# Optimization experiments

Measured on AMD Instinct MI355X. Metric: run time of the kernel, lower is better.

## Reference

```python
import jax, jax.numpy as jnp
import numpy as np

TEMPERATURE = 0.5


def setup_inputs() -> dict:
    key = jax.random.key(0)
    k1, k2 = jax.random.split(key)
    N, D = 4096, 256
    emb_i = jax.random.normal(k1, (N, D), dtype=jnp.float32)
    emb_j = jax.random.normal(k2, (N, D), dtype=jnp.float32)
    return {"emb_i": emb_i, "emb_j": emb_j, "batch_size": N}


def reference(emb_i, emb_j, batch_size):
    N = batch_size
    # L2-normalize each embedding row (F.normalize eps=1e-12)
    def l2n(x):
        return x / jnp.maximum(jnp.linalg.norm(x, axis=1, keepdims=True), 1e-12)
    reps = jnp.concatenate([l2n(emb_i), l2n(emb_j)], axis=0)  # [2N, D]
    # cosine similarity of normalized vectors == dot product
    logits = (reps @ reps.T) / TEMPERATURE                    # [2N, 2N]
    twoN = 2 * N
    # denominator excludes only the self term k != i (stable logsumexp)
    diag_mask = jnp.eye(twoN, dtype=bool)
    masked = jnp.where(diag_mask, -jnp.inf, logits)
    log_denom = jax.nn.logsumexp(masked, axis=1)              # [2N]
    # positive pair for row i is (i+N) mod 2N
    idx = jnp.arange(twoN)
    pos = logits[idx, (idx + N) % twoN]                       # [2N]
    # loss = 1/(2N) * sum_i -log(exp(pos_i)/denom_i)
    return jnp.mean(log_denom - pos)
```

## Files before the change

kernel.cpp:

```cpp
#include <hip/hip_runtime.h>

typedef short short8 __attribute__((ext_vector_type(8)));
typedef float f32x4  __attribute__((ext_vector_type(4)));

#define TWO_N 8192
#define NHALF 4096
#define DDIM  256

__device__ __forceinline__ float b2f(unsigned short u) {
    return __uint_as_float(((unsigned int)u) << 16);
}
__device__ __forceinline__ unsigned short f2b(float f) {
    unsigned int u = __float_as_uint(f);
    u += 0x7fffu + ((u >> 16) & 1u);
    return (unsigned short)(u >> 16);
}

__device__ __forceinline__ int probe_is_f32(const void* p, int lane) {
    unsigned int u = ((const unsigned int*)p)[lane];
    float lowv = __uint_as_float(u << 16);
    int crazy = !(fabsf(lowv) <= 1024.0f);
    return __ballot(crazy) != 0ull;
}

typedef __attribute__((address_space(1))) const unsigned int guint_t;
typedef __attribute__((address_space(3))) unsigned int luint_t;
__device__ __forceinline__ void gl_lds16(const unsigned short* g, unsigned short* l) {
    __builtin_amdgcn_global_load_lds((guint_t*)(const void*)g, (luint_t*)(void*)l, 16, 0, 0);
}

__global__ __launch_bounds__(256) void k_norm(const void* __restrict__ ei,
                                              const void* __restrict__ ej,
                                              unsigned short* __restrict__ reps) {
    int row  = (blockIdx.x * 256 + threadIdx.x) >> 6;
    int lane = threadIdx.x & 63;
    int isf  = probe_is_f32(ei, lane);
    int first = (row < NHALF);
    int r     = first ? row : row - NHALF;
    float x0, x1, x2, x3;
    if (isf) {
        const float* s = (first ? (const float*)ei : (const float*)ej) + (size_t)r * DDIM;
        float4 v = ((const float4*)s)[lane];
        x0 = v.x; x1 = v.y; x2 = v.z; x3 = v.w;
    } else {
        const unsigned short* s =
            (first ? (const unsigned short*)ei : (const unsigned short*)ej) + (size_t)r * DDIM;
        ushort4 v = ((const ushort4*)s)[lane];
        x0 = b2f(v.x); x1 = b2f(v.y); x2 = b2f(v.z); x3 = b2f(v.w);
    }
    float ss = x0 * x0 + x1 * x1 + x2 * x2 + x3 * x3;
    for (int off = 32; off > 0; off >>= 1) ss += __shfl_xor(ss, off);
    float inv = 1.0f / fmaxf(sqrtf(ss), 1e-12f);
    ushort4 o;
    o.x = f2b(x0 * inv); o.y = f2b(x1 * inv);
    o.z = f2b(x2 * inv); o.w = f2b(x3 * inv);
    ((ushort4*)(reps + (size_t)row * DDIM))[lane] = o;
}

__global__ __launch_bounds__(256) void k_main(const unsigned short* __restrict__ R,
                                              float* __restrict__ S_part,
                                              float* __restrict__ pos) {
    __shared__ __align__(16) unsigned short As[128 * 64];
    __shared__ __align__(16) unsigned short Bs[128 * 64];

    int b = blockIdx.x;
    int rb = (int)((129.0f - sqrtf(16641.0f - 8.0f * (float)b)) * 0.5f);
    if (rb > 63) rb = 63;
    while ((129 * (rb + 1) - (rb + 1) * (rb + 1)) / 2 <= b) ++rb;
    while ((129 * rb - rb * rb) / 2 > b) --rb;
    int cb = rb + (b - (129 * rb - rb * rb) / 2);

    const int tid  = threadIdx.x;
    const int wave = tid >> 6;
    const int lane = tid & 63;
    const int quad = lane >> 4;
    const int l16  = lane & 15;
    const int wr   = (wave >> 1) * 64;
    const int wc   = (wave & 1) * 64;
    const int r8   = lane >> 3;
    const int c8   = (lane & 7) ^ r8;

    f32x4 acc[4][4];
#pragma unroll
    for (int r = 0; r < 4; ++r)
#pragma unroll
        for (int c = 0; c < 4; ++c) {
            acc[r][c][0] = 0.0f; acc[r][c][1] = 0.0f;
            acc[r][c][2] = 0.0f; acc[r][c][3] = 0.0f;
        }

    for (int kc = 0; kc < 4; ++kc) {
        __syncthreads();
#pragma unroll
        for (int t = 0; t < 4; ++t) {
            int u = wave * 4 + t;
            const unsigned short* ga =
                R + (size_t)(rb * 128 + u * 8 + r8) * DDIM + kc * 64 + c8 * 8;
            const unsigned short* gb =
                R + (size_t)(cb * 128 + u * 8 + r8) * DDIM + kc * 64 + c8 * 8;
            gl_lds16(ga, &As[u * 512]);
            gl_lds16(gb, &Bs[u * 512]);
        }
        __syncthreads();

#pragma unroll
        for (int kk = 0; kk < 2; ++kk) {
            short8 afr[4], bfr[4];
            int q = kk * 4 + quad;
            int sl = q ^ (l16 & 7);
#pragma unroll
            for (int r = 0; r < 4; ++r)
                afr[r] = *(const short8*)(&As[(wr + r * 16 + l16) * 64 + sl * 8]);
#pragma unroll
            for (int c = 0; c < 4; ++c)
                bfr[c] = *(const short8*)(&Bs[(wc + c * 16 + l16) * 64 + sl * 8]);
#pragma unroll
            for (int r = 0; r < 4; ++r)
#pragma unroll
                for (int c = 0; c < 4; ++c)
                    acc[r][c] = __builtin_amdgcn_mfma_f32_16x16x32_bf16(
                        afr[r], bfr[c], acc[r][c], 0, 0, 0);
        }
    }

    float col_acc[4] = {0.0f, 0.0f, 0.0f, 0.0f};
#pragma unroll
    for (int r = 0; r < 4; ++r)
#pragma unroll
        for (int j = 0; j < 4; ++j) {
            float s = 0.0f;
#pragma unroll
            for (int c = 0; c < 4; ++c) {
                float e = __expf(fmaf(acc[r][c][j], 2.0f, -2.0f));
                s += e;
                col_acc[c] += e;
            }
            s += __shfl_xor(s, 1);
            s += __shfl_xor(s, 2);
            s += __shfl_xor(s, 4);
            s += __shfl_xor(s, 8);
            if (l16 == 0) {
                int row = rb * 128 + wr + r * 16 + quad * 4 + j;
                S_part[(size_t)(2 * cb + (wave & 1)) * TWO_N + row] = s;
            }
        }
    if (rb != cb) {
#pragma unroll
        for (int c = 0; c < 4; ++c) {
            float s = col_acc[c];
            s += __shfl_xor(s, 16);
            s += __shfl_xor(s, 32);
            if (lane < 16) {
                int row = cb * 128 + wc + c * 16 + lane;
                S_part[(size_t)(2 * rb + (wave >> 1)) * TWO_N + row] = s;
            }
        }
    }
    if (cb == rb + 32 && wr == wc) {
#pragma unroll
        for (int r = 0; r < 4; ++r)
#pragma unroll
            for (int j = 0; j < 4; ++j)
                if (quad * 4 + j == l16)
                    pos[rb * 128 + wr + r * 16 + l16] = 2.0f * acc[r][r][j];
    }
}

__global__ __launch_bounds__(256) void k_rows(const float* __restrict__ S_part,
                                              const float* __restrict__ pos,
                                              float* __restrict__ t_row) {
    int row = blockIdx.x * 256 + threadIdx.x;
    float s = 0.0f;
    for (int c = 0; c < 128; ++c) s += S_part[(size_t)c * TWO_N + row];
    float p = (row < NHALF) ? pos[row] : pos[row - NHALF];
    t_row[row] = 2.0f + logf(s - 1.0f) - p;
}

__global__ __launch_bounds__(1024) void k_fin(const float* __restrict__ t_row,
                                              unsigned int* __restrict__ out) {
    int tid = threadIdx.x;
    float local = 0.0f;
    for (int i = tid; i < TWO_N; i += 1024) local += t_row[i];
    __shared__ float red[16];
    for (int off = 32; off > 0; off >>= 1) local += __shfl_xor(local, off);
    if ((tid & 63) == 0) red[tid >> 6] = local;
    __syncthreads();
    if (tid == 0) {
        float v = 0.0f;
        for (int w = 0; w < 16; ++w) v += red[w];
        float L = v / 8192.0f;
        unsigned int bb = (unsigned int)f2b(L);
        out[0] = (bb << 16) | bb;
    }
}

extern "C" void kernel_launch(void* const* d_in, const int* in_sizes, int n_in,
                              void* d_out, int out_size, void* d_ws, size_t ws_size,
                              hipStream_t stream) {
    (void)in_sizes; (void)n_in; (void)out_size; (void)ws_size;
    const void* ei = d_in[0];
    const void* ej = d_in[1];
    char* ws = (char*)d_ws;

    float*          pos    = (float*)(ws);
    float*          t_row  = (float*)(ws + 16384);
    unsigned short* reps   = (unsigned short*)(ws + 49152);
    float*          S_part = (float*)(ws + 4243456);

    k_norm<<<2048, 256, 0, stream>>>(ei, ej, reps);
    k_main<<<2080, 256, 0, stream>>>(reps, S_part, pos);
    k_rows<<<32,   256, 0, stream>>>(S_part, pos, t_row);
    k_fin <<<1,   1024, 0, stream>>>(t_row, (unsigned int*)d_out);
}
```

Before: 110.1 us.

## Fuse row reduction and final loss into main kernel via atomics and last-block

Replaces the per-block partial-sum buffer and two follow-up kernels with float atomicAdds into a per-row accumulator. The last block to finish, found with a global counter, computes the final mean loss. This drops two kernel launches and the 4 MB partial-sum buffer write and read. In exchange it adds atomic contention on the row sums, makes the float summation order nondeterministic, and adds a fence at the end of every block.

```diff
diff --git a/kernel.cpp b/kernel.cpp
--- a/kernel.cpp
+++ b/kernel.cpp
@@ -6,6 +6,7 @@
 #define TWO_N 8192
 #define NHALF 4096
 #define DDIM  256
+#define NBLK  2080
 
 __device__ __forceinline__ float b2f(unsigned short u) {
     return __uint_as_float(((unsigned int)u) << 16);
@@ -31,8 +32,14 @@
 
 __global__ __launch_bounds__(256) void k_norm(const void* __restrict__ ei,
                                               const void* __restrict__ ej,
-                                              unsigned short* __restrict__ reps) {
-    int row  = (blockIdx.x * 256 + threadIdx.x) >> 6;
+                                              unsigned short* __restrict__ reps,
+                                              float* __restrict__ row_acc,
+                                              unsigned int* __restrict__ ctr) {
+    int gid = blockIdx.x * 256 + threadIdx.x;
+    if (gid < TWO_N) row_acc[gid] = 0.0f;
+    if (gid == TWO_N) *ctr = 0u;
+
+    int row  = gid >> 6;
     int lane = threadIdx.x & 63;
     int isf  = probe_is_f32(ei, lane);
     int first = (row < NHALF);
@@ -58,10 +65,14 @@
 }
 
 __global__ __launch_bounds__(256) void k_main(const unsigned short* __restrict__ R,
-                                              float* __restrict__ S_part,
-                                              float* __restrict__ pos) {
+                                              float* __restrict__ row_acc,
+                                              float* __restrict__ pos,
+                                              unsigned int* __restrict__ ctr,
+                                              unsigned int* __restrict__ out) {
     __shared__ __align__(16) unsigned short As[128 * 64];
     __shared__ __align__(16) unsigned short Bs[128 * 64];
+    __shared__ unsigned int sdone;
+    __shared__ float red[4];
 
     int b = blockIdx.x;
     int rb = (int)((129.0f - sqrtf(16641.0f - 8.0f * (float)b)) * 0.5f);
@@ -141,7 +152,7 @@
             s += __shfl_xor(s, 8);
             if (l16 == 0) {
                 int row = rb * 128 + wr + r * 16 + quad * 4 + j;
-                S_part[(size_t)(2 * cb + (wave & 1)) * TWO_N + row] = s;
+                atomicAdd(&row_acc[row], s);
             }
         }
     if (rb != cb) {
@@ -152,7 +163,7 @@
             s += __shfl_xor(s, 32);
             if (lane < 16) {
                 int row = cb * 128 + wc + c * 16 + lane;
-                S_part[(size_t)(2 * rb + (wave >> 1)) * TWO_N + row] = s;
+                atomicAdd(&row_acc[row], s);
             }
         }
     }
@@ -164,33 +175,29 @@
                 if (quad * 4 + j == l16)
                     pos[rb * 128 + wr + r * 16 + l16] = 2.0f * acc[r][r][j];
     }
-}
-
-__global__ __launch_bounds__(256) void k_rows(const float* __restrict__ S_part,
-                                              const float* __restrict__ pos,
-                                              float* __restrict__ t_row) {
-    int row = blockIdx.x * 256 + threadIdx.x;
-    float s = 0.0f;
-    for (int c = 0; c < 128; ++c) s += S_part[(size_t)c * TWO_N + row];
-    float p = (row < NHALF) ? pos[row] : pos[row - NHALF];
-    t_row[row] = 2.0f + logf(s - 1.0f) - p;
-}
-
-__global__ __launch_bounds__(1024) void k_fin(const float* __restrict__ t_row,
-                                              unsigned int* __restrict__ out) {
-    int tid = threadIdx.x;
-    float local = 0.0f;
-    for (int i = tid; i < TWO_N; i += 1024) local += t_row[i];
-    __shared__ float red[16];
-    for (int off = 32; off > 0; off >>= 1) local += __shfl_xor(local, off);
-    if ((tid & 63) == 0) red[tid >> 6] = local;
+
+    __threadfence();
+    if (tid == 0) sdone = atomicAdd(ctr, 1u);
     __syncthreads();
-    if (tid == 0) {
-        float v = 0.0f;
-        for (int w = 0; w < 16; ++w) v += red[w];
-        float L = v / 8192.0f;
-        unsigned int bb = (unsigned int)f2b(L);
-        out[0] = (bb << 16) | bb;
+    if (sdone == NBLK - 1) {
+        __threadfence();
+        float local = 0.0f;
+        for (int i = tid; i < TWO_N; i += 256) {
+            float sv = __hip_atomic_load(&row_acc[i], __ATOMIC_RELAXED,
+                                         __HIP_MEMORY_SCOPE_AGENT);
+            float pv = __hip_atomic_load(&pos[i & (NHALF - 1)], __ATOMIC_RELAXED,
+                                         __HIP_MEMORY_SCOPE_AGENT);
+            local += 2.0f + logf(sv - 1.0f) - pv;
+        }
+        for (int off = 32; off > 0; off >>= 1) local += __shfl_xor(local, off);
+        if ((tid & 63) == 0) red[tid >> 6] = local;
+        __syncthreads();
+        if (tid == 0) {
+            float v = red[0] + red[1] + red[2] + red[3];
+            float L = v / 8192.0f;
+            unsigned int bb = (unsigned int)f2b(L);
+            out[0] = (bb << 16) | bb;
+        }
     }
 }
 
@@ -202,13 +209,11 @@
     const void* ej = d_in[1];
     char* ws = (char*)d_ws;
 
-    float*          pos    = (float*)(ws);
-    float*          t_row  = (float*)(ws + 16384);
-    unsigned short* reps   = (unsigned short*)(ws + 49152);
-    float*          S_part = (float*)(ws + 4243456);
-
-    k_norm<<<2048, 256, 0, stream>>>(ei, ej, reps);
-    k_main<<<2080, 256, 0, stream>>>(reps, S_part, pos);
-    k_rows<<<32,   256, 0, stream>>>(S_part, pos, t_row);
-    k_fin <<<1,   1024, 0, stream>>>(t_row, (unsigned int*)d_out);
-}
+    float*          pos     = (float*)(ws);
+    float*          row_acc = (float*)(ws + 16384);
+    unsigned int*   ctr     = (unsigned int*)(ws + 49152);
+    unsigned short* reps    = (unsigned short*)(ws + 65536);
+
+    k_norm<<<2048, 256, 0, stream>>>(ei, ej, reps, row_acc, ctr);
+    k_main<<<NBLK, 256, 0, stream>>>(reps, row_acc, pos, ctr, (unsigned int*)d_out);
+}
```

New measurement: 232.2 us. +110.9%, slower.
